# Kernel optimization log

Hardware: AMD Instinct MI355X
Metric: run time of the kernel (lower is better)

The kernel has to match this reference:

```python
import jax, jax.numpy as jnp
import numpy as np
from jax import lax

B, C, H, WIN, K = 8, 128, 128, 4, 3
WS = H // 2           # window_size = input_resolution / sqrt(win_num)
L = H * H
DN = ('NCHW', 'OIHW', 'NCHW')


def setup_inputs() -> dict:
    key = jax.random.key(0)
    ks = jax.random.split(key, 12)
    s = 0.02
    return {
        'x': jax.random.normal(ks[0], (B, L, C), jnp.float32),
        # ConvLayer1 params: (win_num*dim, dim, k, k), grouped conv, no bias
        'conv1_w': jax.random.normal(ks[1], (WIN * C, C, K, K), jnp.float32) * s,
        'dc_w': jax.random.normal(ks[2], (WIN, C), jnp.float32) * s,
        'dc_b': jax.random.normal(ks[3], (WIN,), jnp.float32) * s,
        'l1_w': jax.random.normal(ks[4], (4 * WIN, WIN), jnp.float32) * s,
        'l1_b': jax.random.normal(ks[5], (4 * WIN,), jnp.float32) * s,
        'l2_w': jax.random.normal(ks[6], (WIN, 4 * WIN), jnp.float32) * s,
        'l2_b': jax.random.normal(ks[7], (WIN,), jnp.float32) * s,
        'gk_w': jax.random.normal(ks[8], (C, WIN, C), jnp.float32) * s,
        'gk_b': jax.random.normal(ks[9], (C,), jnp.float32) * s,
        'fusion_w': jax.random.normal(ks[10], (C, (WIN + 1) * C), jnp.float32) * s,
        'fusion_b': jax.random.normal(ks[11], (C,), jnp.float32) * s,
    }


def reference(x, conv1_w, dc_w, dc_b, l1_w, l1_b, l2_w, l2_b, gk_w, gk_b, fusion_w, fusion_b):
    Bx = x.shape[0]
    # ka_window_partition: (B, L, C) -> (B, win_num*C, WS, WS), window-major channels
    xw = x.reshape(Bx, 2, WS, 2, WS, C).transpose(0, 1, 3, 5, 2, 4).reshape(Bx, WIN * C, WS, WS)
    # convlayer1: grouped conv, groups=win_num
    wc1 = lax.conv_general_dilated(xw, conv1_w, (1, 1), [(1, 1), (1, 1)],
                                   feature_group_count=WIN, dimension_numbers=DN)
    # SE-style window reweighting
    pooled = wc1.mean(axis=(2, 3)).reshape(Bx, WIN, C)          # adaptive avg pool
    ww = jnp.einsum('bwc,wc->bw', pooled, dc_w) + dc_b          # grouped 1x1 downchannel
    ww = jax.nn.gelu(ww @ l1_w.T + l1_b, approximate=False)
    ww = jax.nn.sigmoid(ww @ l2_w.T + l2_b)
    kern = ww[:, :, None, None, None, None] * conv1_w.reshape(WIN, C, C, K, K)[None]
    gk = jnp.einsum('owj,bwijhk->biohk', gk_w, kern) + gk_b[None, None, :, None, None]
    allk = jnp.concatenate([kern, gk[:, None]], axis=1)
    w_all = allk.reshape(Bx * (WIN + 1) * C, C, K, K)
    ximg = x.reshape(Bx, H, H, C).transpose(0, 3, 1, 2)
    xrep = jnp.tile(ximg, (1, WIN + 1, 1, 1)).reshape(1, Bx * (WIN + 1) * C, H, H)
    y = lax.conv_general_dilated(xrep, w_all, (1, 1), [(1, 1), (1, 1)],
                                 feature_group_count=Bx * (WIN + 1), dimension_numbers=DN)
    y = y.reshape(Bx, (WIN + 1) * C, H, H)
    out = jnp.einsum('oc,bchw->bohw', fusion_w, y) + fusion_b[None, :, None, None]
    return out.transpose(0, 2, 3, 1).reshape(Bx, L, C)
```

## Files before the change

kernel.cpp:

```cpp
#include <hip/hip_runtime.h>
#include <hip/hip_bf16.h>
#include <cmath>

typedef unsigned short u16;
typedef __attribute__((ext_vector_type(8))) short bf16x8;
typedef __attribute__((ext_vector_type(4))) float f32x4;
typedef __attribute__((ext_vector_type(4))) unsigned short u16x4;

#define OFF_AGG   0u
#define OFF_WW    81920u
#define OFF_R     82048u
#define OFF_FSUM  100480u
#define OFF_GKT   100992u
#define OFF_A     363136u
#define OFF_P     2722432u
#define OFF_M     5081728u
#define OFF_KEFF  7441024u
#define OFF_XPAD  9800320u

__device__ __forceinline__ u16 f2bf(float f) {
  union { float f; unsigned int u; } v; v.f = f;
  unsigned int r = v.u + 0x7FFFu + ((v.u >> 16) & 1u);
  return (u16)(r >> 16);
}

__global__ void k1_pad_agg(const float* __restrict__ x, u16* __restrict__ xpad,
                           float* __restrict__ agg) {
  const int rp = blockIdx.x;
  const int b = blockIdx.y;
  const int tid = threadIdx.x;
  const size_t xpb = ((size_t)b * 130 + rp) * 16640;
  if (rp == 0 || rp == 129) {
    const bf16x8 z = {0, 0, 0, 0, 0, 0, 0, 0};
    #pragma unroll
    for (int rr = 0; rr < 8; ++rr)
      *(bf16x8*)(xpad + xpb + (size_t)(rr * 256 + tid) * 8) = z;
    if (tid < 32)
      *(bf16x8*)(xpad + xpb + (size_t)(2048 + tid) * 8) = z;
    return;
  }
  const int r = rp - 1;
  if (tid < 32) {
    *(u16x4*)(xpad + xpb + tid * 4) = (u16x4){0, 0, 0, 0};
  } else if (tid < 64) {
    *(u16x4*)(xpad + xpb + 129 * 128 + (tid - 32) * 4) = (u16x4){0, 0, 0, 0};
  }
  const int s = tid >> 5;
  const int cg = tid & 31;
  const int c0 = cg * 4;
  const float* xr = x + ((size_t)b * 16384 + (size_t)r * 128) * 128;
  f32x4 sum = {0.f, 0.f, 0.f, 0.f};
  f32x4 cap = {0.f, 0.f, 0.f, 0.f};
  #pragma unroll
  for (int qi = 0; qi < 16; ++qi) {
    const int q = s * 16 + qi;
    f32x4 v = *(const f32x4*)(xr + (size_t)q * 128 + c0);
    sum += v;
    if (qi == 0 && (s == 0 || s == 4)) cap = v;
    if (qi == 15 && (s == 3 || s == 7)) cap = v;
    u16x4 st = { f2bf(v[0]), f2bf(v[1]), f2bf(v[2]), f2bf(v[3]) };
    *(u16x4*)(xpad + xpb + (size_t)(q + 1) * 128 + c0) = st;
  }
  const int i = r >> 6, rw = r & 63;
  const int abase = b * 512 + c0;
  if (s == 0) {
    #pragma unroll
    for (int k = 0; k < 4; ++k) atomicAdd(&agg[3 * 4096 + abase + (i * 2) * 128 + k], cap[k]);
  } else if (s == 4) {
    #pragma unroll
    for (int k = 0; k < 4; ++k) atomicAdd(&agg[3 * 4096 + abase + (i * 2 + 1) * 128 + k], cap[k]);
  } else if (s == 3) {
    #pragma unroll
    for (int k = 0; k < 4; ++k) atomicAdd(&agg[4 * 4096 + abase + (i * 2) * 128 + k], cap[k]);
  } else if (s == 7) {
    #pragma unroll
    for (int k = 0; k < 4; ++k) atomicAdd(&agg[4 * 4096 + abase + (i * 2 + 1) * 128 + k], cap[k]);
  }
  __shared__ f32x4 ls[8][32];
  ls[s][cg] = sum;
  __syncthreads();
  if (tid < 64) {
    const int h = tid >> 5, g = tid & 31;
    f32x4 T = ls[h * 4 + 0][g] + ls[h * 4 + 1][g] + ls[h * 4 + 2][g] + ls[h * 4 + 3][g];
    const int a = b * 512 + (i * 2 + h) * 128 + g * 4;
    #pragma unroll
    for (int k = 0; k < 4; ++k) atomicAdd(&agg[a + k], T[k]);
    if (rw == 0) {
      #pragma unroll
      for (int k = 0; k < 4; ++k) atomicAdd(&agg[4096 + a + k], T[k]);
    }
    if (rw == 63) {
      #pragma unroll
      for (int k = 0; k < 4; ++k) atomicAdd(&agg[2 * 4096 + a + k], T[k]);
    }
  }
}

__global__ void kprep(const float* __restrict__ dc_w, const float* __restrict__ conv1_w,
                      const float* __restrict__ gk_w, const float* __restrict__ fusion_w,
                      float* __restrict__ R, float* __restrict__ gkT,
                      float* __restrict__ fsum) {
  const int bid = blockIdx.x, tid = threadIdx.x;
  if (bid < 18) {
    int gid = bid * 256 + tid;
    int w = gid / 1152, m = gid % 1152;
    float s = 0.f;
    for (int o = 0; o < 128; ++o)
      s += dc_w[w * 128 + o] * conv1_w[(size_t)(w * 128 + o) * 1152 + m];
    R[gid] = s;
  } else if (bid < 274) {
    int gid = (bid - 18) * 256 + tid;
    int w = gid >> 14, j = (gid >> 7) & 127, c = gid & 127;
    gkT[gid] = gk_w[c * 512 + w * 128 + j];
  } else if (tid < 128) {
    float s = 0.f;
    for (int oc = 0; oc < 128; ++oc) s += fusion_w[tid * 640 + 512 + oc];
    fsum[tid] = s;
  }
}

__global__ void k2_ww(const float* __restrict__ x, const float* __restrict__ agg,
                      const float* __restrict__ R, const float* __restrict__ dc_b,
                      const float* __restrict__ l1_w, const float* __restrict__ l1_b,
                      const float* __restrict__ l2_w, const float* __restrict__ l2_b,
                      float* __restrict__ ww) {
  const int b = blockIdx.x;
  const int tid = threadIdx.x;
  const int w = tid >> 6, lane = tid & 63;
  __shared__ float red[4];
  float partial = 0.f;
  const int i = w >> 1, j = w & 1;
  const int r0 = i * 64, s0 = j * 64;
  const size_t base = (size_t)b * 16384 * 128;
  #pragma unroll
  for (int k = 0; k < 2; ++k) {
    const int c = lane * 2 + k;
    const int ai = b * 512 + w * 128 + c;
    float T  = agg[ai];
    float rF = agg[4096 + ai];
    float rL = agg[2 * 4096 + ai];
    float cF = agg[3 * 4096 + ai];
    float cL = agg[4 * 4096 + ai];
    float c00 = x[base + ((size_t)(r0 + 0)  * 128 + (s0 + 0))  * 128 + c];
    float c0L = x[base + ((size_t)(r0 + 0)  * 128 + (s0 + 63)) * 128 + c];
    float cL0 = x[base + ((size_t)(r0 + 63) * 128 + (s0 + 0))  * 128 + c];
    float cLL = x[base + ((size_t)(r0 + 63) * 128 + (s0 + 63)) * 128 + c];
    float S[9];
    S[0] = T - rL - cL + cLL;
    S[1] = T - rL;
    S[2] = T - rL - cF + cL0;
    S[3] = T - cL;
    S[4] = T;
    S[5] = T - cF;
    S[6] = T - rF - cL + c0L;
    S[7] = T - rF;
    S[8] = T - rF - cF + c00;
    const float* Rp = R + (w * 128 + c) * 9;
    #pragma unroll
    for (int t = 0; t < 9; ++t) partial += S[t] * Rp[t];
  }
  for (int off = 32; off > 0; off >>= 1) partial += __shfl_xor(partial, off, 64);
  if (lane == 0) red[w] = partial;
  __syncthreads();
  if (tid == 0) {
    float ww0[4];
    #pragma unroll
    for (int w2 = 0; w2 < 4; ++w2) ww0[w2] = red[w2] * (1.f / 4096.f) + dc_b[w2];
    float h1[16];
    for (int i2 = 0; i2 < 16; ++i2) {
      float s = l1_b[i2];
      #pragma unroll
      for (int w2 = 0; w2 < 4; ++w2) s += l1_w[i2 * 4 + w2] * ww0[w2];
      h1[i2] = 0.5f * s * (1.f + erff(s * 0.70710678118654752f));
    }
    for (int w2 = 0; w2 < 4; ++w2) {
      float s = l2_b[w2];
      for (int i2 = 0; i2 < 16; ++i2) s += l2_w[w2 * 16 + i2] * h1[i2];
      ww[b * 4 + w2] = 1.f / (1.f + expf(-s));
    }
  }
}

__global__ void k3_AP(const float* __restrict__ fusion_w, const float* __restrict__ conv1_w,
                      float* __restrict__ A, float* __restrict__ P) {
  int gid = blockIdx.x * 256 + threadIdx.x;
  int w = gid / 36864;
  int rem = gid % 36864;
  int o = rem / 288;
  int m = (rem % 288) * 4;
  const float* fw1 = fusion_w + o * 640 + w * 128;
  const float* fw4 = fusion_w + o * 640 + 512;
  const float* cw = conv1_w + (size_t)w * 128 * 1152 + m;
  float a0 = 0, a1 = 0, a2 = 0, a3 = 0, p0 = 0, p1 = 0, p2 = 0, p3 = 0;
  for (int oc = 0; oc < 128; ++oc) {
    float f1 = fw1[oc], f4 = fw4[oc];
    float4 cv = *(const float4*)(cw + (size_t)oc * 1152);
    a0 += f1 * cv.x; a1 += f1 * cv.y; a2 += f1 * cv.z; a3 += f1 * cv.w;
    p0 += f4 * cv.x; p1 += f4 * cv.y; p2 += f4 * cv.z; p3 += f4 * cv.w;
  }
  float4* Ao = (float4*)(A + (size_t)(w * 128 + o) * 1152 + m);
  float4* Po = (float4*)(P + (size_t)(w * 128 + o) * 1152 + m);
  *Ao = make_float4(a0, a1, a2, a3);
  *Po = make_float4(p0, p1, p2, p3);
}

__global__ void k45_keff(const float* __restrict__ A, const float* __restrict__ P,
                         const float* __restrict__ gkT, const float* __restrict__ ww,
                         const float* __restrict__ fsum, const float* __restrict__ gk_b,
                         u16* __restrict__ keff) {
  const int t = blockIdx.x >> 6;
  const int o0 = (blockIdx.x & 63) * 2;
  const int tid = threadIdx.x;
  __shared__ float pl[2][4][128];
  __shared__ float al[2][4][128];
  __shared__ float red[2][2][4][128];
  #pragma unroll
  for (int rr = 0; rr < 4; ++rr) {
    const int idx = rr * 256 + tid;
    const int oi = idx >> 9, w = (idx >> 7) & 3, j = idx & 127;
    const size_t src = (size_t)(w * 128 + o0 + oi) * 1152 + j * 9 + t;
    pl[oi][w][j] = P[src];
    al[oi][w][j] = A[src];
  }
  __syncthreads();
  const int c = tid & 127, jh = tid >> 7;
  float acc[2][4];
  #pragma unroll
  for (int oi = 0; oi < 2; ++oi)
    #pragma unroll
    for (int w = 0; w < 4; ++w) acc[oi][w] = 0.f;
  const float* g = gkT + c;
  #pragma unroll 4
  for (int j = jh * 64; j < jh * 64 + 64; ++j) {
    const float g0 = g[0 * 16384 + j * 128];
    const float g1 = g[1 * 16384 + j * 128];
    const float g2 = g[2 * 16384 + j * 128];
    const float g3 = g[3 * 16384 + j * 128];
    #pragma unroll
    for (int oi = 0; oi < 2; ++oi) {
      acc[oi][0] += pl[oi][0][j] * g0;
      acc[oi][1] += pl[oi][1][j] * g1;
      acc[oi][2] += pl[oi][2][j] * g2;
      acc[oi][3] += pl[oi][3][j] * g3;
    }
  }
  #pragma unroll
  for (int oi = 0; oi < 2; ++oi)
    #pragma unroll
    for (int w = 0; w < 4; ++w) red[jh][oi][w][c] = acc[oi][w];
  __syncthreads();
  const int oi2 = tid >> 7, c2 = tid & 127;
  float m[4];
  #pragma unroll
  for (int w = 0; w < 4; ++w)
    m[w] = red[0][oi2][w][c2] + red[1][oi2][w][c2] + al[oi2][w][c2];
  const float base = fsum[o0 + oi2] * gk_b[c2];
  #pragma unroll
  for (int b = 0; b < 8; ++b) {
    float r = base;
    #pragma unroll
    for (int w = 0; w < 4; ++w) r += ww[b * 4 + w] * m[w];
    keff[(size_t)b * 147456 + (size_t)t * 16384 + (o0 + oi2) * 128 + c2] = f2bf(r);
  }
}

__global__ __launch_bounds__(256, 2) void k6_conv(
    const u16* __restrict__ xpad, const u16* __restrict__ keff,
    const float* __restrict__ fusion_b, float* __restrict__ out) {
  __shared__ __align__(16) u16 alds[130 * 128];
  __shared__ __align__(16) u16 apad[256];
  __shared__ __align__(16) u16 wlds[128 * 128];
  const int tid = threadIdx.x;
  const int blk = blockIdx.x;
  const int b = blk & 7;
  const int p = blk >> 3;
  const int wid = tid >> 6;
  const int lane = tid & 63;
  const int wm = (wid & 1) * 64;
  const int wn = (wid >> 1) * 64;
  const int quad = lane >> 4;
  const int l16 = lane & 15;

  f32x4 acc[4][4];
  #pragma unroll
  for (int i = 0; i < 4; ++i)
    #pragma unroll
    for (int j = 0; j < 4; ++j)
      acc[i][j] = (f32x4){0.f, 0.f, 0.f, 0.f};

  const u16* kb = keff + (size_t)b * 147456;
  const u16* xb = xpad + (size_t)b * 130 * 16640;
  bf16x8 streg[8];
  (void)apad;

  auto stage_W_load = [&](int tap) {
    const u16* src = kb + tap * 16384;
    #pragma unroll
    for (int it = 0; it < 8; ++it) {
      const int chunk = it * 256 + tid;
      const int gs = chunk ^ ((chunk >> 4) & 7);
      streg[it] = *(const bf16x8*)(src + gs * 8);
    }
  };
  auto stage_W_write = [&]() {
    #pragma unroll
    for (int it = 0; it < 8; ++it)
      *(bf16x8*)(wlds + (it * 256 + tid) * 8) = streg[it];
  };
  auto stage_A_dma = [&](int prow) {
    const u16* src = xb + (size_t)prow * 16640;
    #pragma unroll
    for (int r = 0; r < 8; ++r) {
      const int chunk = (wid * 8 + r) * 64 + lane;
      const int gs = chunk ^ ((chunk >> 4) & 7);
      __builtin_amdgcn_global_load_lds(
          (const __attribute__((address_space(1))) unsigned int*)(src + (size_t)gs * 8),
          (__attribute__((address_space(3))) unsigned int*)(alds + (wid * 8 + r) * 512),
          16, 0, 0);
    }
    if (tid < 32) {
      const int chunk = 2048 + tid;
      const int gs = chunk ^ ((chunk >> 4) & 7);
      __builtin_amdgcn_global_load_lds(
          (const __attribute__((address_space(1))) unsigned int*)(src + (size_t)gs * 8),
          (__attribute__((address_space(3))) unsigned int*)(alds + 2048 * 8),
          16, 0, 0);
    }
  };

  stage_W_load(0);
  stage_A_dma(p);
  stage_W_write();
  __syncthreads();

  for (int tap = 0; tap < 9; ++tap) {
    if (tap < 8) stage_W_load(tap + 1);
    const int dw = tap % 3 - 1;
    const int pixoff = 1 + dw;
    #pragma unroll
    for (int kc = 0; kc < 4; ++kc) {
      const int c0 = kc * 32 + quad * 8;
      bf16x8 a[4], bb[4];
      #pragma unroll
      for (int i = 0; i < 4; ++i) {
        const int pix = pixoff + wm + i * 16 + l16;
        const int off = (pix * 128 + c0) ^ ((pix & 7) << 3);
        a[i] = *(const bf16x8*)(alds + off);
      }
      #pragma unroll
      for (int j = 0; j < 4; ++j) {
        const int row = wn + j * 16 + l16;
        const int off = (row * 128 + c0) ^ ((row & 7) << 3);
        bb[j] = *(const bf16x8*)(wlds + off);
      }
      #pragma unroll
      for (int i = 0; i < 4; ++i)
        #pragma unroll
        for (int j = 0; j < 4; ++j)
          acc[i][j] = __builtin_amdgcn_mfma_f32_16x16x32_bf16(a[i], bb[j], acc[i][j], 0, 0, 0);
    }
    __syncthreads();
    if (tap < 8) {
      stage_W_write();
      if (tap % 3 == 2) stage_A_dma(p + (tap + 1) / 3);
      __syncthreads();
    }
  }

  float fb[4];
  #pragma unroll
  for (int j = 0; j < 4; ++j) fb[j] = fusion_b[wn + j * 16 + l16];
  float* outb = out + ((size_t)b * 16384 + (size_t)p * 128) * 128;
  #pragma unroll
  for (int i = 0; i < 4; ++i)
    #pragma unroll
    for (int r = 0; r < 4; ++r) {
      const int m = wm + i * 16 + quad * 4 + r;
      #pragma unroll
      for (int j = 0; j < 4; ++j)
        outb[(size_t)m * 128 + (wn + j * 16 + l16)] = acc[i][j][r] + fb[j];
    }
}

extern "C" void kernel_launch(void* const* d_in, const int* in_sizes, int n_in,
                              void* d_out, int out_size, void* d_ws, size_t ws_size,
                              hipStream_t stream) {
  const float* x        = (const float*)d_in[0];
  const float* conv1_w  = (const float*)d_in[1];
  const float* dc_w     = (const float*)d_in[2];
  const float* dc_b     = (const float*)d_in[3];
  const float* l1_w     = (const float*)d_in[4];
  const float* l1_b     = (const float*)d_in[5];
  const float* l2_w     = (const float*)d_in[6];
  const float* l2_b     = (const float*)d_in[7];
  const float* gk_w     = (const float*)d_in[8];
  const float* gk_b     = (const float*)d_in[9];
  const float* fusion_w = (const float*)d_in[10];
  const float* fusion_b = (const float*)d_in[11];
  float* out = (float*)d_out;
  char* ws = (char*)d_ws;

  float* agg  = (float*)(ws + OFF_AGG);
  float* ww   = (float*)(ws + OFF_WW);
  float* R    = (float*)(ws + OFF_R);
  float* fsum = (float*)(ws + OFF_FSUM);
  float* gkT  = (float*)(ws + OFF_GKT);
  float* A    = (float*)(ws + OFF_A);
  float* P    = (float*)(ws + OFF_P);
  u16* keff   = (u16*)(ws + OFF_KEFF);
  u16* xpad   = (u16*)(ws + OFF_XPAD);

  hipMemsetAsync(agg, 0, 81920, stream);
  k1_pad_agg<<<dim3(130, 8), 256, 0, stream>>>(x, xpad, agg);
  kprep<<<275, 256, 0, stream>>>(dc_w, conv1_w, gk_w, fusion_w, R, gkT, fsum);
  k2_ww<<<8, 256, 0, stream>>>(x, agg, R, dc_b, l1_w, l1_b, l2_w, l2_b, ww);
  k3_AP<<<576, 256, 0, stream>>>(fusion_w, conv1_w, A, P);
  k45_keff<<<576, 256, 0, stream>>>(A, P, gkT, ww, fsum, gk_b, keff);
  k6_conv<<<1024, 256, 0, stream>>>(xpad, keff, fusion_b, out);
}
```

Baseline: 246.1 us.

## Merge prep kernels and fold window reweighting into keff kernel

Merges the agg memset, kprep and k3_AP weight products into a single launch, and moves the SE-style window-weight computation (k2_ww) into every k45_keff block, which recomputes it redundantly. This cuts the pipeline from seven launches to four, removing launch gaps and serialization. The gkT contraction in k45_keff is also rewritten to use float4 loads with a four-way j split. The cost is that each of the 576 keff blocks now redoes the ww reduction, reading agg and x corner values.

```diff
diff --git a/kernel.cpp b/kernel.cpp
--- a/kernel.cpp
+++ b/kernel.cpp
@@ -22,6 +22,58 @@
   union { float f; unsigned int u; } v; v.f = f;
   unsigned int r = v.u + 0x7FFFu + ((v.u >> 16) & 1u);
   return (u16)(r >> 16);
+}
+
+__global__ void kw(const float* __restrict__ dc_w, const float* __restrict__ conv1_w,
+                   const float* __restrict__ gk_w, const float* __restrict__ fusion_w,
+                   float* __restrict__ R, float* __restrict__ gkT,
+                   float* __restrict__ fsum, float* __restrict__ agg,
+                   float* __restrict__ A, float* __restrict__ P) {
+  const int bid = blockIdx.x, tid = threadIdx.x;
+  if (bid < 18) {
+    int gid = bid * 256 + tid;
+    int w = gid / 1152, m = gid % 1152;
+    float s = 0.f;
+    for (int o = 0; o < 128; ++o)
+      s += dc_w[w * 128 + o] * conv1_w[(size_t)(w * 128 + o) * 1152 + m];
+    R[gid] = s;
+  } else if (bid < 274) {
+    int gid = (bid - 18) * 256 + tid;
+    int w = gid >> 14, j = (gid >> 7) & 127, c = gid & 127;
+    gkT[gid] = gk_w[c * 512 + w * 128 + j];
+  } else if (bid == 274) {
+    if (tid < 128) {
+      float s = 0.f;
+      for (int oc = 0; oc < 128; ++oc) s += fusion_w[tid * 640 + 512 + oc];
+      fsum[tid] = s;
+    }
+  } else if (bid < 279) {
+    const int idx = (bid - 275) * 256 + tid;
+    f32x4 z = {0.f, 0.f, 0.f, 0.f};
+    #pragma unroll
+    for (int k = 0; k < 5; ++k)
+      *(f32x4*)(agg + idx * 20 + k * 4) = z;
+  } else {
+    int gid = (bid - 279) * 256 + tid;
+    int w = gid / 36864;
+    int rem = gid % 36864;
+    int o = rem / 288;
+    int m = (rem % 288) * 4;
+    const float* fw1 = fusion_w + o * 640 + w * 128;
+    const float* fw4 = fusion_w + o * 640 + 512;
+    const float* cw = conv1_w + (size_t)w * 128 * 1152 + m;
+    float a0 = 0, a1 = 0, a2 = 0, a3 = 0, p0 = 0, p1 = 0, p2 = 0, p3 = 0;
+    for (int oc = 0; oc < 128; ++oc) {
+      float f1 = fw1[oc], f4 = fw4[oc];
+      float4 cv = *(const float4*)(cw + (size_t)oc * 1152);
+      a0 += f1 * cv.x; a1 += f1 * cv.y; a2 += f1 * cv.z; a3 += f1 * cv.w;
+      p0 += f4 * cv.x; p1 += f4 * cv.y; p2 += f4 * cv.z; p3 += f4 * cv.w;
+    }
+    float4* Ao = (float4*)(A + (size_t)(w * 128 + o) * 1152 + m);
+    float4* Po = (float4*)(P + (size_t)(w * 128 + o) * 1152 + m);
+    *Ao = make_float4(a0, a1, a2, a3);
+    *Po = make_float4(p0, p1, p2, p3);
+  }
 }
 
 __global__ void k1_pad_agg(const float* __restrict__ x, u16* __restrict__ xpad,
@@ -96,116 +148,12 @@
   }
 }
 
-__global__ void kprep(const float* __restrict__ dc_w, const float* __restrict__ conv1_w,
-                      const float* __restrict__ gk_w, const float* __restrict__ fusion_w,
-                      float* __restrict__ R, float* __restrict__ gkT,
-                      float* __restrict__ fsum) {
-  const int bid = blockIdx.x, tid = threadIdx.x;
-  if (bid < 18) {
-    int gid = bid * 256 + tid;
-    int w = gid / 1152, m = gid % 1152;
-    float s = 0.f;
-    for (int o = 0; o < 128; ++o)
-      s += dc_w[w * 128 + o] * conv1_w[(size_t)(w * 128 + o) * 1152 + m];
-    R[gid] = s;
-  } else if (bid < 274) {
-    int gid = (bid - 18) * 256 + tid;
-    int w = gid >> 14, j = (gid >> 7) & 127, c = gid & 127;
-    gkT[gid] = gk_w[c * 512 + w * 128 + j];
-  } else if (tid < 128) {
-    float s = 0.f;
-    for (int oc = 0; oc < 128; ++oc) s += fusion_w[tid * 640 + 512 + oc];
-    fsum[tid] = s;
-  }
-}
-
-__global__ void k2_ww(const float* __restrict__ x, const float* __restrict__ agg,
-                      const float* __restrict__ R, const float* __restrict__ dc_b,
-                      const float* __restrict__ l1_w, const float* __restrict__ l1_b,
-                      const float* __restrict__ l2_w, const float* __restrict__ l2_b,
-                      float* __restrict__ ww) {
-  const int b = blockIdx.x;
-  const int tid = threadIdx.x;
-  const int w = tid >> 6, lane = tid & 63;
-  __shared__ float red[4];
-  float partial = 0.f;
-  const int i = w >> 1, j = w & 1;
-  const int r0 = i * 64, s0 = j * 64;
-  const size_t base = (size_t)b * 16384 * 128;
-  #pragma unroll
-  for (int k = 0; k < 2; ++k) {
-    const int c = lane * 2 + k;
-    const int ai = b * 512 + w * 128 + c;
-    float T  = agg[ai];
-    float rF = agg[4096 + ai];
-    float rL = agg[2 * 4096 + ai];
-    float cF = agg[3 * 4096 + ai];
-    float cL = agg[4 * 4096 + ai];
-    float c00 = x[base + ((size_t)(r0 + 0)  * 128 + (s0 + 0))  * 128 + c];
-    float c0L = x[base + ((size_t)(r0 + 0)  * 128 + (s0 + 63)) * 128 + c];
-    float cL0 = x[base + ((size_t)(r0 + 63) * 128 + (s0 + 0))  * 128 + c];
-    float cLL = x[base + ((size_t)(r0 + 63) * 128 + (s0 + 63)) * 128 + c];
-    float S[9];
-    S[0] = T - rL - cL + cLL;
-    S[1] = T - rL;
-    S[2] = T - rL - cF + cL0;
-    S[3] = T - cL;
-    S[4] = T;
-    S[5] = T - cF;
-    S[6] = T - rF - cL + c0L;
-    S[7] = T - rF;
-    S[8] = T - rF - cF + c00;
-    const float* Rp = R + (w * 128 + c) * 9;
-    #pragma unroll
-    for (int t = 0; t < 9; ++t) partial += S[t] * Rp[t];
-  }
-  for (int off = 32; off > 0; off >>= 1) partial += __shfl_xor(partial, off, 64);
-  if (lane == 0) red[w] = partial;
-  __syncthreads();
-  if (tid == 0) {
-    float ww0[4];
-    #pragma unroll
-    for (int w2 = 0; w2 < 4; ++w2) ww0[w2] = red[w2] * (1.f / 4096.f) + dc_b[w2];
-    float h1[16];
-    for (int i2 = 0; i2 < 16; ++i2) {
-      float s = l1_b[i2];
-      #pragma unroll
-      for (int w2 = 0; w2 < 4; ++w2) s += l1_w[i2 * 4 + w2] * ww0[w2];
-      h1[i2] = 0.5f * s * (1.f + erff(s * 0.70710678118654752f));
-    }
-    for (int w2 = 0; w2 < 4; ++w2) {
-      float s = l2_b[w2];
-      for (int i2 = 0; i2 < 16; ++i2) s += l2_w[w2 * 16 + i2] * h1[i2];
-      ww[b * 4 + w2] = 1.f / (1.f + expf(-s));
-    }
-  }
-}
-
-__global__ void k3_AP(const float* __restrict__ fusion_w, const float* __restrict__ conv1_w,
-                      float* __restrict__ A, float* __restrict__ P) {
-  int gid = blockIdx.x * 256 + threadIdx.x;
-  int w = gid / 36864;
-  int rem = gid % 36864;
-  int o = rem / 288;
-  int m = (rem % 288) * 4;
-  const float* fw1 = fusion_w + o * 640 + w * 128;
-  const float* fw4 = fusion_w + o * 640 + 512;
-  const float* cw = conv1_w + (size_t)w * 128 * 1152 + m;
-  float a0 = 0, a1 = 0, a2 = 0, a3 = 0, p0 = 0, p1 = 0, p2 = 0, p3 = 0;
-  for (int oc = 0; oc < 128; ++oc) {
-    float f1 = fw1[oc], f4 = fw4[oc];
-    float4 cv = *(const float4*)(cw + (size_t)oc * 1152);
-    a0 += f1 * cv.x; a1 += f1 * cv.y; a2 += f1 * cv.z; a3 += f1 * cv.w;
-    p0 += f4 * cv.x; p1 += f4 * cv.y; p2 += f4 * cv.z; p3 += f4 * cv.w;
-  }
-  float4* Ao = (float4*)(A + (size_t)(w * 128 + o) * 1152 + m);
-  float4* Po = (float4*)(P + (size_t)(w * 128 + o) * 1152 + m);
-  *Ao = make_float4(a0, a1, a2, a3);
-  *Po = make_float4(p0, p1, p2, p3);
-}
-
 __global__ void k45_keff(const float* __restrict__ A, const float* __restrict__ P,
-                         const float* __restrict__ gkT, const float* __restrict__ ww,
+                         const float* __restrict__ gkT, const float* __restrict__ agg,
+                         const float* __restrict__ x, const float* __restrict__ R,
+                         const float* __restrict__ dc_b,
+                         const float* __restrict__ l1_w, const float* __restrict__ l1_b,
+                         const float* __restrict__ l2_w, const float* __restrict__ l2_b,
                          const float* __restrict__ fsum, const float* __restrict__ gk_b,
                          u16* __restrict__ keff) {
   const int t = blockIdx.x >> 6;
@@ -213,7 +161,10 @@
   const int tid = threadIdx.x;
   __shared__ float pl[2][4][128];
   __shared__ float al[2][4][128];
-  __shared__ float red[2][2][4][128];
+  __shared__ float red[4][2][4][128];
+  __shared__ float redw[8][4];
+  __shared__ float ww_l[8][4];
+
   #pragma unroll
   for (int rr = 0; rr < 4; ++rr) {
     const int idx = rr * 256 + tid;
@@ -222,45 +173,106 @@
     pl[oi][w][j] = P[src];
     al[oi][w][j] = A[src];
   }
+
+  {
+    const int g8 = tid >> 3;
+    const int b = g8 >> 2, w = g8 & 3;
+    const int l8 = tid & 7;
+    const int iw = w >> 1, jw = w & 1;
+    const int r0 = iw * 64, s0 = jw * 64;
+    const size_t xbase = (size_t)b * 16384 * 128;
+    float partial = 0.f;
+    for (int k = 0; k < 16; ++k) {
+      const int c = l8 * 16 + k;
+      const int ai = b * 512 + w * 128 + c;
+      float T  = agg[ai];
+      float rF = agg[4096 + ai];
+      float rL = agg[2 * 4096 + ai];
+      float cF = agg[3 * 4096 + ai];
+      float cL = agg[4 * 4096 + ai];
+      float c00 = x[xbase + ((size_t)(r0 + 0)  * 128 + (s0 + 0))  * 128 + c];
+      float c0L = x[xbase + ((size_t)(r0 + 0)  * 128 + (s0 + 63)) * 128 + c];
+      float cL0 = x[xbase + ((size_t)(r0 + 63) * 128 + (s0 + 0))  * 128 + c];
+      float cLL = x[xbase + ((size_t)(r0 + 63) * 128 + (s0 + 63)) * 128 + c];
+      float S[9];
+      S[0] = T - rL - cL + cLL;
+      S[1] = T - rL;
+      S[2] = T - rL - cF + cL0;
+      S[3] = T - cL;
+      S[4] = T;
+      S[5] = T - cF;
+      S[6] = T - rF - cL + c0L;
+      S[7] = T - rF;
+      S[8] = T - rF - cF + c00;
+      const float* Rp = R + (w * 128 + c) * 9;
+      #pragma unroll
+      for (int tt = 0; tt < 9; ++tt) partial += S[tt] * Rp[tt];
+    }
+    #pragma unroll
+    for (int off = 4; off > 0; off >>= 1) partial += __shfl_xor(partial, off, 8);
+    if (l8 == 0) redw[b][w] = partial;
+  }
   __syncthreads();
-  const int c = tid & 127, jh = tid >> 7;
-  float acc[2][4];
-  #pragma unroll
-  for (int oi = 0; oi < 2; ++oi)
-    #pragma unroll
-    for (int w = 0; w < 4; ++w) acc[oi][w] = 0.f;
-  const float* g = gkT + c;
-  #pragma unroll 4
-  for (int j = jh * 64; j < jh * 64 + 64; ++j) {
-    const float g0 = g[0 * 16384 + j * 128];
-    const float g1 = g[1 * 16384 + j * 128];
-    const float g2 = g[2 * 16384 + j * 128];
-    const float g3 = g[3 * 16384 + j * 128];
-    #pragma unroll
-    for (int oi = 0; oi < 2; ++oi) {
-      acc[oi][0] += pl[oi][0][j] * g0;
-      acc[oi][1] += pl[oi][1][j] * g1;
-      acc[oi][2] += pl[oi][2][j] * g2;
-      acc[oi][3] += pl[oi][3][j] * g3;
-    }
-  }
-  #pragma unroll
-  for (int oi = 0; oi < 2; ++oi)
-    #pragma unroll
-    for (int w = 0; w < 4; ++w) red[jh][oi][w][c] = acc[oi][w];
+
+  if (tid < 8) {
+    const int b = tid;
+    float ww0[4];
+    #pragma unroll
+    for (int w2 = 0; w2 < 4; ++w2) ww0[w2] = redw[b][w2] * (1.f / 4096.f) + dc_b[w2];
+    float h1[16];
+    for (int i2 = 0; i2 < 16; ++i2) {
+      float s = l1_b[i2];
+      #pragma unroll
+      for (int w2 = 0; w2 < 4; ++w2) s += l1_w[i2 * 4 + w2] * ww0[w2];
+      h1[i2] = 0.5f * s * (1.f + erff(s * 0.70710678118654752f));
+    }
+    #pragma unroll
+    for (int w2 = 0; w2 < 4; ++w2) {
+      float s = l2_b[w2];
+      for (int i2 = 0; i2 < 16; ++i2) s += l2_w[w2 * 16 + i2] * h1[i2];
+      ww_l[b][w2] = 1.f / (1.f + expf(-s));
+    }
+  }
+
+  {
+    const int cq = tid & 31;
+    const int oi = (tid >> 5) & 1;
+    const int jq = tid >> 6;
+    f32x4 acc0 = {0,0,0,0}, acc1 = {0,0,0,0}, acc2 = {0,0,0,0}, acc3 = {0,0,0,0};
+    const float* gbase = gkT + cq * 4;
+    for (int j5 = 0; j5 < 32; ++j5) {
+      const int j = jq * 32 + j5;
+      f32x4 g0 = *(const f32x4*)(gbase + 0 * 16384 + j * 128);
+      f32x4 g1 = *(const f32x4*)(gbase + 1 * 16384 + j * 128);
+      f32x4 g2 = *(const f32x4*)(gbase + 2 * 16384 + j * 128);
+      f32x4 g3 = *(const f32x4*)(gbase + 3 * 16384 + j * 128);
+      acc0 += pl[oi][0][j] * g0;
+      acc1 += pl[oi][1][j] * g1;
+      acc2 += pl[oi][2][j] * g2;
+      acc3 += pl[oi][3][j] * g3;
+    }
+    *(f32x4*)&red[jq][oi][0][cq * 4] = acc0;
+    *(f32x4*)&red[jq][oi][1][cq * 4] = acc1;
+    *(f32x4*)&red[jq][oi][2][cq * 4] = acc2;
+    *(f32x4*)&red[jq][oi][3][cq * 4] = acc3;
+  }
   __syncthreads();
-  const int oi2 = tid >> 7, c2 = tid & 127;
-  float m[4];
-  #pragma unroll
-  for (int w = 0; w < 4; ++w)
-    m[w] = red[0][oi2][w][c2] + red[1][oi2][w][c2] + al[oi2][w][c2];
-  const float base = fsum[o0 + oi2] * gk_b[c2];
-  #pragma unroll
-  for (int b = 0; b < 8; ++b) {
-    float r = base;
-    #pragma unroll
-    for (int w = 0; w < 4; ++w) r += ww[b * 4 + w] * m[w];
-    keff[(size_t)b * 147456 + (size_t)t * 16384 + (o0 + oi2) * 128 + c2] = f2bf(r);
+
+  {
+    const int oi2 = tid >> 7, c2 = tid & 127;
+    float m[4];
+    #pragma unroll
+    for (int w = 0; w < 4; ++w)
+      m[w] = red[0][oi2][w][c2] + red[1][oi2][w][c2] + red[2][oi2][w][c2]
+           + red[3][oi2][w][c2] + al[oi2][w][c2];
+    const float base = fsum[o0 + oi2] * gk_b[c2];
+    #pragma unroll
+    for (int b = 0; b < 8; ++b) {
+      float r = base;
+      #pragma unroll
+      for (int w = 0; w < 4; ++w) r += ww_l[b][w] * m[w];
+      keff[(size_t)b * 147456 + (size_t)t * 16384 + (o0 + oi2) * 128 + c2] = f2bf(r);
+    }
   }
 }
 
@@ -401,7 +413,6 @@
   char* ws = (char*)d_ws;
 
   float* agg  = (float*)(ws + OFF_AGG);
-  float* ww   = (float*)(ws + OFF_WW);
   float* R    = (float*)(ws + OFF_R);
   float* fsum = (float*)(ws + OFF_FSUM);
   float* gkT  = (float*)(ws + OFF_GKT);
@@ -410,11 +421,9 @@
   u16* keff   = (u16*)(ws + OFF_KEFF);
   u16* xpad   = (u16*)(ws + OFF_XPAD);
 
-  hipMemsetAsync(agg, 0, 81920, stream);
+  kw<<<855, 256, 0, stream>>>(dc_w, conv1_w, gk_w, fusion_w, R, gkT, fsum, agg, A, P);
   k1_pad_agg<<<dim3(130, 8), 256, 0, stream>>>(x, xpad, agg);
-  kprep<<<275, 256, 0, stream>>>(dc_w, conv1_w, gk_w, fusion_w, R, gkT, fsum);
-  k2_ww<<<8, 256, 0, stream>>>(x, agg, R, dc_b, l1_w, l1_b, l2_w, l2_b, ww);
-  k3_AP<<<576, 256, 0, stream>>>(fusion_w, conv1_w, A, P);
-  k45_keff<<<576, 256, 0, stream>>>(A, P, gkT, ww, fsum, gk_b, keff);
+  k45_keff<<<576, 256, 0, stream>>>(A, P, gkT, agg, x, R, dc_b,
+                                    l1_w, l1_b, l2_w, l2_b, fsum, gk_b, keff);
   k6_conv<<<1024, 256, 0, stream>>>(xpad, keff, fusion_b, out);
 }
```

New measurement: 269.6 us. 1.1x slower.
